# Kernel tuning notes

Hardware: AMD Instinct MI355X
Metric: run time of the kernel (lower is better)

The kernel has to match this reference:

```python
import jax, jax.numpy as jnp
import numpy as np

L1 = 512
LX = 32
COUNT = 8


def setup_inputs() -> dict:
    key = jax.random.key(0)
    ks = jax.random.split(key, 9)
    B = 65536
    x = jax.random.uniform(ks[0], (B, 2 * L1), dtype=jnp.float32)  # NNUE accumulator is in [0,1]
    ls_indices = jax.random.randint(ks[1], (B,), 0, COUNT, dtype=jnp.int64)
    # params (scaled ~1/sqrt(fan_in))
    w_fact = jax.random.normal(ks[2], (LX, 2 * L1), dtype=jnp.float32) * (1.0 / np.sqrt(2 * L1))
    w0 = jax.random.normal(ks[3], (LX * COUNT, 2 * L1), dtype=jnp.float32) * (1.0 / np.sqrt(2 * L1))
    b0 = jax.random.normal(ks[4], (LX * COUNT,), dtype=jnp.float32) * 0.05
    w1 = jax.random.normal(ks[5], (LX * COUNT, LX), dtype=jnp.float32) * (1.0 / np.sqrt(LX))
    b1 = jax.random.normal(ks[6], (LX * COUNT,), dtype=jnp.float32) * 0.05
    w2 = jax.random.normal(ks[7], (1 * COUNT, LX), dtype=jnp.float32) * (1.0 / np.sqrt(LX))
    b2 = jax.random.normal(ks[8], (1 * COUNT,), dtype=jnp.float32) * 0.05
    return {"x": x, "ls_indices": ls_indices, "w_fact": w_fact,
            "w0": w0, "b0": b0, "w1": w1, "b1": b1, "w2": w2, "b2": b2}


def _stack_linear_gather(h, w, b, idx, out_dim):
    # dense Linear for all COUNT buckets, then gather the selected bucket per row
    y = (h @ w.T + b).reshape(-1, COUNT, out_dim)          # [B, COUNT, out_dim]
    return y.reshape(-1, out_dim)[idx]                      # [B, out_dim]


def reference(x, ls_indices, w_fact, w0, b0, w1, b1, w2, b2):
    B = x.shape[0]
    idx = ls_indices.astype(jnp.int32) + jnp.arange(B, dtype=jnp.int32) * COUNT
    l1f = x @ w_fact.T                                      # [B, LX]
    h = _stack_linear_gather(x, w0, b0, idx, LX) + l1f      # layer 0 + factorized term
    h = jnp.clip(h, 0.0, 1.0)
    h = _stack_linear_gather(h, w1, b1, idx, LX)            # hidden layer 1
    h = jnp.clip(h, 0.0, 1.0)
    out = _stack_linear_gather(h, w2, b2, idx, 1)           # output layer (no clamp)
    return out
```

## Files before the change

kernel.cpp:

```cpp
#include <hip/hip_runtime.h>


#define B_ROWS 65536
#define LK     1024
#define TILE   32
#define NBLK   (B_ROWS / TILE)
#define SROW   2056


typedef short  short8  __attribute__((ext_vector_type(8)));
typedef float  f32x16  __attribute__((ext_vector_type(16)));

__device__ __forceinline__ unsigned pkbf(float a, float b) {
    unsigned ua = __float_as_uint(a), ub = __float_as_uint(b);
    ua = (ua + 0x7FFFu + ((ua >> 16) & 1u)) >> 16;
    ub = (ub + 0x7FFFu + ((ub >> 16) & 1u)) >> 16;
    return (ua & 0xFFFFu) | (ub << 16);
}

__device__ __forceinline__ bool detect_i64(const int* p) {
    int acc = 0;
#pragma unroll
    for (int i = 0; i < 64; ++i) acc |= p[2 * i + 1];
    return acc == 0;
}

__device__ __forceinline__ int load_bucket(const int* p, int r, bool i64) {
    return (i64 ? p[2 * r] : p[r]) & 7;
}

__global__ __launch_bounds__(1024) void k_prep(
    const float* __restrict__ w0, const float* __restrict__ wf,
    uint4* __restrict__ wB)
{
    int f = blockIdx.x * 1024 + threadIdx.x;
    int b   = f >> 12;
    int i12 = f & 4095;
    int kc  = i12 >> 8;
    int i8  = i12 & 255;
    int n   = i8 & 31;
    int khi = i8 >> 5;
    int k = kc * 64 + khi * 8;
    const float* p0 = w0 + (size_t)(b * 32 + n) * LK + k;
    const float* pf = wf + (size_t)n * LK + k;
    float v[8];
#pragma unroll
    for (int j = 0; j < 8; ++j) v[j] = p0[j] + pf[j];
    uint4 o;
    o.x = pkbf(v[0], v[1]); o.y = pkbf(v[2], v[3]);
    o.z = pkbf(v[4], v[5]); o.w = pkbf(v[6], v[7]);
    wB[f] = o;
}

__global__ __launch_bounds__(256, 2) void k_main(
    const float* __restrict__ x, const int* __restrict__ idx,
    const uint4* __restrict__ wB, const float* __restrict__ b0,
    const float* __restrict__ w1, const float* __restrict__ b1,
    const float* __restrict__ w2, const float* __restrict__ b2,
    float* __restrict__ out)
{
    __shared__ __align__(16) unsigned char smem[TILE * SROW];
    __shared__ float hb[TILE * 36];
    __shared__ int   bkt_s[TILE];

    int row0 = blockIdx.x * TILE;
    int t    = threadIdx.x;
    int lane = t & 63;
    int wv   = t >> 6;

    if (t < TILE) {
        bool i64 = detect_i64(idx);
        bkt_s[t] = load_bucket(idx, row0 + t, i64);
    }

#pragma unroll
    for (int j0 = 0; j0 < 32; j0 += 8) {
        float4 v[8];
#pragma unroll
        for (int jj = 0; jj < 8; ++jj)
            v[jj] = ((const float4*)(x + (size_t)(row0 + j0 + jj) * LK))[t];
#pragma unroll
        for (int jj = 0; jj < 8; ++jj) {
            uint2 o;
            o.x = pkbf(v[jj].x, v[jj].y);
            o.y = pkbf(v[jj].z, v[jj].w);
            *(uint2*)(smem + (j0 + jj) * SROW + t * 8) = o;
        }
    }
    __syncthreads();

    const uint4* wB0 = wB + (size_t)(2 * wv) * 4096;
    const uint4* wB1 = wB + (size_t)(2 * wv + 1) * 4096;
    const unsigned char* Abase = smem + (size_t)(lane & 31) * SROW + 16 * (lane >> 5);

    f32x16 acc0, acc1;
#pragma unroll
    for (int i = 0; i < 16; ++i) { acc0[i] = 0.0f; acc1[i] = 0.0f; }

    union UA { uint2 h[2]; short8 s; };
    union UB { uint4 u;    short8 s; };
#pragma unroll 4
    for (int c = 0; c < 64; ++c) {
        UA ua;
        ua.h[0] = *(const uint2*)(Abase + 32 * c);
        ua.h[1] = *(const uint2*)(Abase + 32 * c + 8);
        UB ub0, ub1;
        ub0.u = wB0[c * 64 + lane];
        ub1.u = wB1[c * 64 + lane];
        acc0 = __builtin_amdgcn_mfma_f32_32x32x16_bf16(ua.s, ub0.s, acc0, 0, 0, 0);
        acc1 = __builtin_amdgcn_mfma_f32_32x32x16_bf16(ua.s, ub1.s, acc1, 0, 0, 0);
    }

    int bb0 = 2 * wv, bb1 = 2 * wv + 1;
#pragma unroll
    for (int i = 0; i < 16; ++i) {
        int m = (i & 3) + 8 * (i >> 2) + 4 * (lane >> 5);
        int n = lane & 31;
        int mb = bkt_s[m];
        if (mb == bb0 || mb == bb1) {
            float s = (mb == bb0) ? acc0[i] : acc1[i];
            float h = s + b0[mb * 32 + n];
            hb[m * 36 + n] = fminf(fmaxf(h, 0.0f), 1.0f);
        }
    }
    __syncthreads();

    if (t < 64) {
        int r = t >> 1, half = t & 1;
        int bkt = bkt_s[r];
        const float4* hr = (const float4*)(hb + r * 36);
        float4 ha[8];
#pragma unroll
        for (int q = 0; q < 8; ++q) ha[q] = hr[q];
        const float* w1b = w1 + (size_t)bkt * 1024;
        const float* b1b = b1 + bkt * 32;
        const float* w2b = w2 + bkt * 32;
        float partial = 0.0f;
#pragma unroll
        for (int jj = 0; jj < 16; ++jj) {
            int j2 = half * 16 + jj;
            const float4* wr = (const float4*)&w1b[j2 * 32];
            float s = b1b[j2];
#pragma unroll
            for (int q = 0; q < 8; ++q) {
                float4 w4 = wr[q];
                s += ha[q].x * w4.x + ha[q].y * w4.y + ha[q].z * w4.z + ha[q].w * w4.w;
            }
            s = fminf(fmaxf(s, 0.0f), 1.0f);
            partial += s * w2b[j2];
        }
        partial += __shfl_xor(partial, 1);
        if (half == 0) out[row0 + r] = partial + b2[bkt];
    }
}

extern "C" void kernel_launch(void* const* d_in, const int* in_sizes, int n_in,
                              void* d_out, int out_size, void* d_ws, size_t ws_size,
                              hipStream_t stream) {
    const float* x   = (const float*)d_in[0];
    const int*   lsi = (const int*)  d_in[1];
    const float* wf  = (const float*)d_in[2];
    const float* w0  = (const float*)d_in[3];
    const float* b0  = (const float*)d_in[4];
    const float* w1  = (const float*)d_in[5];
    const float* b1  = (const float*)d_in[6];
    const float* w2  = (const float*)d_in[7];
    const float* b2  = (const float*)d_in[8];
    float* out = (float*)d_out;

    uint4* wB = (uint4*)d_ws;

    k_prep<<<32, 1024, 0, stream>>>(w0, wf, wB);
    k_main<<<NBLK, 256, 0, stream>>>(x, lsi, wB, b0, w1, b1, w2, b2, out);
}
```

Baseline: 451.8 us.

## Load x directly from global into MFMA operands, drop LDS staging

Removes the shared-memory staging of the bf16-converted x tile. Each wave now reads its A fragments straight from global memory and converts them with the hardware v_cvt_pk_bf16_f32 instruction. With the large LDS buffer gone, launch bounds are raised so more blocks can be resident per CU. The trade-off is that all four waves load the same x rows, so each block reads x from global four times, relying on cache to absorb the redundancy. The loads are also strided per lane.

```diff
diff --git a/kernel.cpp b/kernel.cpp
--- a/kernel.cpp
+++ b/kernel.cpp
@@ -5,7 +5,6 @@
 #define LK     1024
 #define TILE   32
 #define NBLK   (B_ROWS / TILE)
-#define SROW   2056
 
 
 typedef short  short8  __attribute__((ext_vector_type(8)));
@@ -16,6 +15,12 @@
     ua = (ua + 0x7FFFu + ((ua >> 16) & 1u)) >> 16;
     ub = (ub + 0x7FFFu + ((ub >> 16) & 1u)) >> 16;
     return (ua & 0xFFFFu) | (ub << 16);
+}
+
+__device__ __forceinline__ unsigned cvtpk(float a, float b) {
+    unsigned r;
+    asm("v_cvt_pk_bf16_f32 %0, %1, %2" : "=v"(r) : "v"(a), "v"(b));
+    return r;
 }
 
 __device__ __forceinline__ bool detect_i64(const int* p) {
@@ -52,14 +57,13 @@
     wB[f] = o;
 }
 
-__global__ __launch_bounds__(256, 2) void k_main(
+__global__ __launch_bounds__(256, 4) void k_main(
     const float* __restrict__ x, const int* __restrict__ idx,
     const uint4* __restrict__ wB, const float* __restrict__ b0,
     const float* __restrict__ w1, const float* __restrict__ b1,
     const float* __restrict__ w2, const float* __restrict__ b2,
     float* __restrict__ out)
 {
-    __shared__ __align__(16) unsigned char smem[TILE * SROW];
     __shared__ float hb[TILE * 36];
     __shared__ int   bkt_s[TILE];
 
@@ -72,41 +76,30 @@
         bool i64 = detect_i64(idx);
         bkt_s[t] = load_bucket(idx, row0 + t, i64);
     }
-
-#pragma unroll
-    for (int j0 = 0; j0 < 32; j0 += 8) {
-        float4 v[8];
-#pragma unroll
-        for (int jj = 0; jj < 8; ++jj)
-            v[jj] = ((const float4*)(x + (size_t)(row0 + j0 + jj) * LK))[t];
-#pragma unroll
-        for (int jj = 0; jj < 8; ++jj) {
-            uint2 o;
-            o.x = pkbf(v[jj].x, v[jj].y);
-            o.y = pkbf(v[jj].z, v[jj].w);
-            *(uint2*)(smem + (j0 + jj) * SROW + t * 8) = o;
-        }
-    }
     __syncthreads();
 
     const uint4* wB0 = wB + (size_t)(2 * wv) * 4096;
-    const uint4* wB1 = wB + (size_t)(2 * wv + 1) * 4096;
-    const unsigned char* Abase = smem + (size_t)(lane & 31) * SROW + 16 * (lane >> 5);
+    const uint4* wB1 = wB0 + 4096;
+    const float* Ab  = x + (size_t)(row0 + (lane & 31)) * LK + (lane >> 5) * 8;
 
     f32x16 acc0, acc1;
 #pragma unroll
     for (int i = 0; i < 16; ++i) { acc0[i] = 0.0f; acc1[i] = 0.0f; }
 
-    union UA { uint2 h[2]; short8 s; };
-    union UB { uint4 u;    short8 s; };
+    union UA { uint4 u; short8 s; };
+    union UB { uint4 u; short8 s; };
 #pragma unroll 4
     for (int c = 0; c < 64; ++c) {
-        UA ua;
-        ua.h[0] = *(const uint2*)(Abase + 32 * c);
-        ua.h[1] = *(const uint2*)(Abase + 32 * c + 8);
+        float4 a0 = *(const float4*)(Ab + c * 16);
+        float4 a1 = *(const float4*)(Ab + c * 16 + 4);
         UB ub0, ub1;
         ub0.u = wB0[c * 64 + lane];
         ub1.u = wB1[c * 64 + lane];
+        UA ua;
+        ua.u.x = cvtpk(a0.x, a0.y);
+        ua.u.y = cvtpk(a0.z, a0.w);
+        ua.u.z = cvtpk(a1.x, a1.y);
+        ua.u.w = cvtpk(a1.z, a1.w);
         acc0 = __builtin_amdgcn_mfma_f32_32x32x16_bf16(ua.s, ub0.s, acc0, 0, 0, 0);
         acc1 = __builtin_amdgcn_mfma_f32_32x32x16_bf16(ua.s, ub1.s, acc1, 0, 0, 0);
     }
```

Measured after the change: 513.3 us. +13.6%, slower.
